# Optimization experiments

Hardware: AMD Instinct MI355X
Metric: run time of the kernel (lower is better)

The kernel has to match this reference:

```python
import jax, jax.numpy as jnp
import numpy as np

D_STATE = 16
D_CONV = 4
EXPAND = 2
GROUPS = 8
EPS = 1e-5


def _layernorm(x, w, b):
    m = x.mean(-1, keepdims=True)
    v = x.var(-1, keepdims=True)
    return (x - m) * jax.lax.rsqrt(v + EPS) * w + b


def _groupnorm(x, w, b):
    B, C = x.shape[:2]
    sp = x.shape[2:]
    xg = x.reshape(B, GROUPS, C // GROUPS, -1)
    m = xg.mean(axis=(2, 3), keepdims=True)
    v = xg.var(axis=(2, 3), keepdims=True)
    xg = (xg - m) * jax.lax.rsqrt(v + EPS)
    x = xg.reshape((B, C) + sp)
    shp = (1, C) + (1,) * len(sp)
    return x * w.reshape(shp) + b.reshape(shp)


def _mamba(xn, in_w, conv_w, conv_b, xp_w, dt_w, dt_b, A_log, Dp, out_w):
    # xn: [B, L, C]
    B, L, C = xn.shape
    di = in_w.shape[0] // 2
    rank = dt_w.shape[1]
    N = D_STATE
    xz = xn @ in_w.T                              # [B, L, 2*di]
    xi, z = xz[..., :di], xz[..., di:]
    # causal depthwise conv1d along L (pad left d_conv-1, truncate to L)
    xc = jnp.moveaxis(xi, 1, 2)                   # [B, di, L]
    xpd = jnp.pad(xc, ((0, 0), (0, 0), (D_CONV - 1, 0)))
    conv = conv_b[None, :, None]
    for k in range(D_CONV):
        conv = conv + conv_w[None, :, k, None] * xpd[:, :, k:k + L]
    u = jnp.moveaxis(jax.nn.silu(conv), 1, 2)     # [B, L, di]
    dbl = u @ xp_w.T                              # [B, L, rank+2N]
    dt = dbl[..., :rank]
    Bm = dbl[..., rank:rank + N]
    Cm = dbl[..., rank + N:]
    delta = jax.nn.softplus(dt @ dt_w.T + dt_b)   # [B, L, di]
    A = -jnp.exp(A_log)                           # [di, N]
    dA = jnp.exp(delta[..., None] * A)            # [B, L, di, N]
    dBu = delta[..., None] * Bm[:, :, None, :] * u[..., None]

    def comb(e1, e2):
        a1, b1 = e1
        a2, b2 = e2
        return a1 * a2, a2 * b1 + b2

    _, h = jax.lax.associative_scan(comb, (dA, dBu), axis=1)  # h_t = dA_t*h_{t-1} + dBu_t
    y = jnp.einsum('bldn,bln->bld', h, Cm) + u * Dp
    y = y * jax.nn.silu(z)
    return y @ out_w.T


def _mamba_layer(x, p):
    B, C = x.shape[:2]
    img = x.shape[2:]
    L = int(np.prod(img))
    xf = jnp.moveaxis(x.reshape(B, C, L), 1, 2)   # [B, L, C]
    xn = _layernorm(xf, p['ln_w'], p['ln_b'])
    xm = _mamba(xn, p['in_w'], p['conv_w'], p['conv_b'], p['xp_w'],
                p['dt_w'], p['dt_b'], p['A_log'], p['Dp'], p['out_w'])
    xm = xm + p['skip'] * xf
    xm = _layernorm(xm, p['ln_w'], p['ln_b'])     # same norm params reused, as in source
    y = xm @ p['proj_w'].T + p['proj_b']
    return jnp.moveaxis(y, 1, 2).reshape((B, C) + img)


def setup_inputs() -> dict:
    key = jax.random.key(0)
    B, C = 2, 48
    img = (16, 32, 32)
    di = EXPAND * C
    rank = -(-C // 16)
    ks = iter(jax.random.split(key, 64))

    def nrm(shape, scale):
        return jax.random.normal(next(ks), shape, jnp.float32) * scale

    inp = {'x': jax.random.normal(next(ks), (B, C) + img, jnp.float32)}
    inp['gn1_w'] = jnp.ones(C); inp['gn1_b'] = jnp.zeros(C)
    inp['gn2_w'] = jnp.ones(C); inp['gn2_b'] = jnp.zeros(C)
    for i in (1, 2):
        inp[f'ln{i}_w'] = jnp.ones(C); inp[f'ln{i}_b'] = jnp.zeros(C)
        inp[f'in_w{i}'] = nrm((2 * di, C), C ** -0.5)
        inp[f'conv_w{i}'] = nrm((di, D_CONV), D_CONV ** -0.5)
        inp[f'conv_b{i}'] = jnp.zeros(di)
        inp[f'xp_w{i}'] = nrm((rank + 2 * D_STATE, di), di ** -0.5)
        inp[f'dt_w{i}'] = nrm((di, rank), rank ** -0.5)
        inp[f'dt_b{i}'] = nrm((di,), 0.1) - 4.0  # softplus -> small positive dt
        inp[f'A_log{i}'] = jnp.log(jnp.tile(jnp.arange(1, D_STATE + 1, dtype=jnp.float32), (di, 1)))
        inp[f'D{i}'] = jnp.ones(di)
        inp[f'out_w{i}'] = nrm((C, di), di ** -0.5)
        inp[f'proj_w{i}'] = nrm((C, C), C ** -0.5)
        inp[f'proj_b{i}'] = jnp.zeros(C)
        inp[f'skip{i}'] = jnp.ones(1)
    return inp


def reference(x, gn1_w, gn1_b, gn2_w, gn2_b,
              ln1_w, ln1_b, in_w1, conv_w1, conv_b1, xp_w1, dt_w1, dt_b1, A_log1, D1, out_w1, proj_w1, proj_b1, skip1,
              ln2_w, ln2_b, in_w2, conv_w2, conv_b2, xp_w2, dt_w2, dt_b2, A_log2, D2, out_w2, proj_w2, proj_b2, skip2):
    p1 = dict(ln_w=ln1_w, ln_b=ln1_b, in_w=in_w1, conv_w=conv_w1, conv_b=conv_b1, xp_w=xp_w1,
              dt_w=dt_w1, dt_b=dt_b1, A_log=A_log1, Dp=D1, out_w=out_w1, proj_w=proj_w1,
              proj_b=proj_b1, skip=skip1)
    p2 = dict(ln_w=ln2_w, ln_b=ln2_b, in_w=in_w2, conv_w=conv_w2, conv_b=conv_b2, xp_w=xp_w2,
              dt_w=dt_w2, dt_b=dt_b2, A_log=A_log2, Dp=D2, out_w=out_w2, proj_w=proj_w2,
              proj_b=proj_b2, skip=skip2)
    identity = x
    h = jax.nn.relu(_groupnorm(x, gn1_w, gn1_b))
    h = _mamba_layer(h, p1)
    h = jax.nn.relu(_groupnorm(h, gn2_w, gn2_b))
    h = _mamba_layer(h, p2)
    return h + identity
```

## Files before the change

### kernel.cpp

```cpp
#include <hip/hip_runtime.h>
#include <hip/hip_bf16.h>

#define LCH   48
#define DI    96
#define LSEQ  16384
#define NB    2
#define NPOS  (NB*LSEQ)
#define NSTATE 16
#define CPG   6
#define EPS   1e-5f
#define NC    128
#define CL    128
#define NCHAIN (NB*DI*NSTATE)
#define TS    32

typedef __hip_bfloat16 bf16;

__device__ __forceinline__ float LDW(const void* p, size_t i, bool f32){
    return f32 ? ((const float*)p)[i] : __bfloat162float(((const bf16*)p)[i]);
}

__device__ __forceinline__ float bf2f(unsigned short h){
    union { unsigned int i; float f; } u; u.i = ((unsigned int)h) << 16; return u.f;
}

__device__ __forceinline__ float4 LDW4(const void* p, size_t i4, bool f32){
    if (f32) return ((const float4*)p)[i4];
    ushort4 v = ((const ushort4*)p)[i4];
    return make_float4(bf2f(v.x), bf2f(v.y), bf2f(v.z), bf2f(v.w));
}

__device__ __forceinline__ float row16_sum(float p){
    union { float f; int i; } u, v;
    u.f = p; v.i = __builtin_amdgcn_mov_dpp(u.i, 0x111, 0xf, 0xf, true); p += v.f;
    u.f = p; v.i = __builtin_amdgcn_mov_dpp(u.i, 0x112, 0xf, 0xf, true); p += v.f;
    u.f = p; v.i = __builtin_amdgcn_mov_dpp(u.i, 0x114, 0xf, 0xf, true); p += v.f;
    u.f = p; v.i = __builtin_amdgcn_mov_dpp(u.i, 0x118, 0xf, 0xf, true); p += v.f;
    return p;
}

__global__ void k_flag(const void* gnw, int* flag, float* __restrict__ acc1, float* __restrict__ acc2){
    int t = threadIdx.x;
    if (t == 0){
        const unsigned short* g = (const unsigned short*)gnw;
        flag[0] = (g[0] == 0x3F80) ? 0 : 1;
    }
    if (t < 32){ acc1[t] = 0.f; acc2[t] = 0.f; }
}

__global__ void k_gnpart_x(const void* __restrict__ x, const int* Fg, float* __restrict__ acc){
    const bool f32 = Fg[0];
    int bg = blockIdx.x >> 4, sl = blockIdx.x & 15;
    int b = bg >> 3, g = bg & 7;
    int tid = threadIdx.x;
    float s = 0.f, q = 0.f;
    for (int c = 0; c < CPG; ++c){
        size_t base = (size_t)(b*LCH + g*CPG + c)*LSEQ + sl*1024;
        float4 v = LDW4(x, base/4 + tid, f32);
        s += v.x; q += v.x*v.x;
        s += v.y; q += v.y*v.y;
        s += v.z; q += v.z*v.z;
        s += v.w; q += v.w*v.w;
    }
    __shared__ float ss[256], sq[256];
    ss[tid] = s; sq[tid] = q; __syncthreads();
    for (int st = 128; st > 0; st >>= 1){
        if (tid < st){ ss[tid] += ss[tid+st]; sq[tid] += sq[tid+st]; }
        __syncthreads();
    }
    if (tid == 0){
        atomicAdd(&acc[bg*2],   ss[0]);
        atomicAdd(&acc[bg*2+1], sq[0]);
    }
}

template<int SRC>
__global__ void k_prepin(const void* __restrict__ src, const int* Fg, const float* __restrict__ acc,
                         const void* gnw, const void* gnb, const void* lnw, const void* lnb,
                         const void* __restrict__ inw,
                         float* __restrict__ xf, float* __restrict__ xi, float* __restrict__ z){
    const bool f32 = Fg[0];
    __shared__ float wl[96*52];
    __shared__ float xl[32*52];
    __shared__ float fl[32*52];
    __shared__ float sst[32];
    int tid = threadIdx.x;
    int part = blockIdx.x & 1;
    int pos0 = (blockIdx.x >> 1)*32;
    int b = pos0 >> 14, l0 = pos0 & (LSEQ-1);
    if (tid < 16){
        float mean = acc[tid*2] / (float)(CPG*LSEQ);
        float var  = acc[tid*2+1] / (float)(CPG*LSEQ) - mean*mean;
        sst[tid*2]   = mean;
        sst[tid*2+1] = rsqrtf(var + EPS);
    }
    for (int i = tid; i < 96*12; i += 256){
        int o = i/12, k4 = i - o*12;
        ((float4*)wl)[o*13+k4] = LDW4(inw, (size_t)part*1152 + i, f32);
    }
    if (SRC == 0){
        for (int i = tid; i < 48*32; i += 256){
            int c = i >> 5, p = i & 31;
            xl[p*52+c] = LDW(src, (size_t)(b*LCH+c)*LSEQ + l0 + p, f32);
        }
    } else {
        const float4* ms4 = (const float4*)src;
        for (int i = tid; i < 32*12; i += 256){
            int p = i/12, c4 = i - p*12;
            ((float4*)xl)[p*13+c4] = ms4[(size_t)pos0*12 + i];
        }
    }
    __syncthreads();
    if (tid < 32){
        float* row  = xl + tid*52;
        float* frow = fl + tid*52;
        float s = 0.f, q = 0.f;
        #pragma unroll
        for (int c = 0; c < LCH; ++c){
            int g = c / CPG;
            float mean = sst[(b*8+g)*2], rs = sst[(b*8+g)*2+1];
            float v = row[c];
            v = (v - mean)*rs*LDW(gnw,c,f32) + LDW(gnb,c,f32);
            v = fmaxf(v, 0.f);
            frow[c] = v; s += v; q += v*v;
        }
        float mean = s / (float)LCH;
        float rs = rsqrtf(q/(float)LCH - mean*mean + EPS);
        #pragma unroll
        for (int c = 0; c < LCH; ++c)
            row[c] = (frow[c]-mean)*rs*LDW(lnw,c,f32) + LDW(lnb,c,f32);
    }
    __syncthreads();
    if (part == 0){
        float4* xf4 = (float4*)xf;
        const float4* fl4 = (const float4*)fl;
        for (int i = tid; i < 32*12; i += 256){
            int p = i/12, c4 = i - p*12;
            xf4[(size_t)pos0*12 + i] = fl4[p*13+c4];
        }
    }
    float* dst = part ? z : xi;
    int o  = tid & 31;
    int pg = tid >> 5;
    const float4* wl4 = (const float4*)wl;
    const float4* xl4 = (const float4*)xl;
    float a0[4] = {0.f,0.f,0.f,0.f};
    float a1[4] = {0.f,0.f,0.f,0.f};
    float a2[4] = {0.f,0.f,0.f,0.f};
    #pragma unroll
    for (int k4 = 0; k4 < 12; ++k4){
        float4 w0 = wl4[ o     *13 + k4];
        float4 w1 = wl4[(o+32)*13 + k4];
        float4 w2 = wl4[(o+64)*13 + k4];
        #pragma unroll
        for (int q = 0; q < 4; ++q){
            float4 xv = xl4[(pg*4+q)*13 + k4];
            a0[q] += xv.x*w0.x; a0[q] += xv.y*w0.y; a0[q] += xv.z*w0.z; a0[q] += xv.w*w0.w;
            a1[q] += xv.x*w1.x; a1[q] += xv.y*w1.y; a1[q] += xv.z*w1.z; a1[q] += xv.w*w1.w;
            a2[q] += xv.x*w2.x; a2[q] += xv.y*w2.y; a2[q] += xv.z*w2.z; a2[q] += xv.w*w2.w;
        }
    }
    #pragma unroll
    for (int q = 0; q < 4; ++q){
        size_t pos = (size_t)(pos0 + pg*4 + q);
        dst[pos*DI + o     ] = a0[q];
        dst[pos*DI + o + 32] = a1[q];
        dst[pos*DI + o + 64] = a2[q];
    }
}

__global__ void k_convdbl(const float* __restrict__ xi, const void* cw, const void* cb,
                          const void* __restrict__ xpw, const void* dtw, const void* dtb,
                          const int* Fg, float* __restrict__ u_g, float* __restrict__ BC2,
                          float* __restrict__ delta_g){
    const bool f32 = Fg[0];
    __shared__ float xil[35*100];
    __shared__ float wbc[32*100];
    __shared__ float wdt[3*100];
    __shared__ float cwl[96*4];
    __shared__ float cbl[96];
    __shared__ float dtwl[96*3];
    __shared__ float dtbl[96];
    __shared__ float dtl[32*3];
    int tid = threadIdx.x;
    int pos0 = blockIdx.x*32;
    int l0 = pos0 & (LSEQ-1);

    for (int i = tid; i < 32*24; i += 256){
        int o = i/24, k4 = i - o*24;
        int row = (o & 1) ? (19 + (o>>1)) : (3 + (o>>1));
        ((float4*)wbc)[o*25 + k4] = LDW4(xpw, (size_t)row*24 + k4, f32);
    }
    if (tid < 72){
        int o = tid/24, k4 = tid - o*24;
        ((float4*)wdt)[o*25 + k4] = LDW4(xpw, (size_t)o*24 + k4, f32);
    }
    for (int i = tid; i < 96*4; i += 256) cwl[i] = LDW(cw, i, f32);
    if (tid < 96) cbl[tid] = LDW(cb, tid, f32);
    for (int i = tid; i < 96*3; i += 256) dtwl[i] = LDW(dtw, i, f32);
    if (tid >= 128 && tid < 224) dtbl[tid-128] = LDW(dtb, tid-128, f32);
    {
        float4* xv = (float4*)xil;
        const float4* gx = (const float4*)xi;
        for (int i = tid; i < 35*24; i += 256){
            int p = i/24, k4 = i - p*24;
            float4 v = make_float4(0.f, 0.f, 0.f, 0.f);
            if (l0 + p - 3 >= 0) v = gx[(size_t)(pos0-3+p)*24 + k4];
            xv[p*25 + k4] = v;
        }
    }
    __syncthreads();

    float uu[12];
    #pragma unroll
    for (int r = 0; r < 12; ++r){
        int i = tid + 256*r;
        int j = i/96, d = i - j*96;
        float4 cw4 = ((const float4*)cwl)[d];
        float acc = cbl[d];
        acc += cw4.x*xil[(j+0)*100+d];
        acc += cw4.y*xil[(j+1)*100+d];
        acc += cw4.z*xil[(j+2)*100+d];
        acc += cw4.w*xil[(j+3)*100+d];
        uu[r] = acc / (1.f + __expf(-acc));
    }
    __syncthreads();

    #pragma unroll
    for (int r = 0; r < 12; ++r){
        int i = tid + 256*r;
        int j = i/96, d = i - j*96;
        xil[j*100+d] = uu[r];
        u_g[(size_t)pos0*DI + i] = uu[r];
    }
    __syncthreads();

    {
        int o  = tid & 31;
        int pg = ((tid>>6)<<1) | ((tid>>5)&1);
        const float4* ulv = (const float4*)xil;
        const float4* wv  = (const float4*)wbc;
        float a0=0.f, a1=0.f, a2=0.f, a3=0.f;
        #pragma unroll 4
        for (int k4 = 0; k4 < 24; ++k4){
            float4 u0 = ulv[(pg*4+0)*25 + k4];
            float4 u1 = ulv[(pg*4+1)*25 + k4];
            float4 u2 = ulv[(pg*4+2)*25 + k4];
            float4 u3 = ulv[(pg*4+3)*25 + k4];
            float4 w  = wv[o*25 + k4];
            a0 += u0.x*w.x; a0 += u0.y*w.y; a0 += u0.z*w.z; a0 += u0.w*w.w;
            a1 += u1.x*w.x; a1 += u1.y*w.y; a1 += u1.z*w.z; a1 += u1.w*w.w;
            a2 += u2.x*w.x; a2 += u2.y*w.y; a2 += u2.z*w.z; a2 += u2.w*w.w;
            a3 += u3.x*w.x; a3 += u3.y*w.y; a3 += u3.z*w.z; a3 += u3.w*w.w;
        }
        size_t pb = (size_t)(pos0 + pg*4);
        BC2[(pb+0)*32 + o] = a0;
        BC2[(pb+1)*32 + o] = a1;
        BC2[(pb+2)*32 + o] = a2;
        BC2[(pb+3)*32 + o] = a3;
    }
    if (tid < 96){
        int o = tid >> 5;
        int p = tid & 31;
        const float4* ulv = (const float4*)xil;
        const float4* wv  = (const float4*)wdt;
        float a = 0.f;
        #pragma unroll 4
        for (int k4 = 0; k4 < 24; ++k4){
            float4 uv = ulv[p*25 + k4];
            float4 w  = wv[o*25 + k4];
            a += uv.x*w.x; a += uv.y*w.y; a += uv.z*w.z; a += uv.w*w.w;
        }
        dtl[p*3+o] = a;
    }
    __syncthreads();

    for (int i = tid; i < 32*96; i += 256){
        int p = i/96, d = i - p*96;
        float acc = dtbl[d];
        #pragma unroll
        for (int r = 0; r < 3; ++r) acc += dtl[p*3+r]*dtwl[d*3+r];
        float sp = (acc > 20.f) ? acc : log1pf(__expf(acc));
        delta_g[(size_t)pos0*DI + i] = sp;
    }
}

__global__ void k_scanA(const float* __restrict__ delta, const float* __restrict__ u,
                        const float* __restrict__ BC2, const void* Alog, const int* Fg,
                        float* __restrict__ Pb, float* __restrict__ Sb){
    const bool f32 = Fg[0];
    __shared__ float  dls[2][TS*16];
    __shared__ float  uus[2][TS*16];
    __shared__ float2 bcs[2][TS*16];
    int tid = threadIdx.x;
    int t = blockIdx.x*256 + tid;
    int n = tid & 15;
    int sg0 = blockIdx.x*16;
    int cb2 = sg0/96;
    int d0 = sg0 - cb2*96;
    int b = cb2 & 1, chunk = cb2 >> 1;
    int dloc = tid >> 4;
    int d = d0 + dloc;
    float An = -__expf(LDW(Alog, d*16+n, f32));
    float P = 1.f, S = 0.f;
    int base = b*LSEQ + chunk*CL;
    const float2* BC2v = (const float2*)BC2;
    int si0 = tid >> 4, sj = tid & 15;
    int si1 = si0 + 16;
    float pd0, pd1, pu0, pu1; float2 pb0, pb1;
    auto fetch = [&](int tb){
        pd0 = delta[(size_t)(tb+si0)*DI + d0 + sj];
        pu0 = u    [(size_t)(tb+si0)*DI + d0 + sj];
        pb0 = BC2v [(size_t)(tb+si0)*16 + sj];
        pd1 = delta[(size_t)(tb+si1)*DI + d0 + sj];
        pu1 = u    [(size_t)(tb+si1)*DI + d0 + sj];
        pb1 = BC2v [(size_t)(tb+si1)*16 + sj];
    };
    auto store = [&](int bs){
        dls[bs][tid] = pd0; dls[bs][tid+256] = pd1;
        uus[bs][tid] = pu0; uus[bs][tid+256] = pu1;
        bcs[bs][tid] = pb0; bcs[bs][tid+256] = pb1;
    };
    fetch(base); store(0);
    __syncthreads();
    for (int tile = 0; tile < CL/TS; ++tile){
        int cur = tile & 1;
        if (tile+1 < CL/TS) fetch(base + (tile+1)*TS);
        #pragma unroll
        for (int i = 0; i < TS; ++i){
            float dl = dls[cur][i*16 + dloc];
            float uu = uus[cur][i*16 + dloc];
            float Bn = bcs[cur][i*16 + n].x;
            float a = __expf(dl*An);
            P *= a;
            S = a*S + dl*Bn*uu;
        }
        if (tile+1 < CL/TS) store(1-cur);
        __syncthreads();
    }
    Pb[t] = P; Sb[t] = S;
}

__global__ void k_scanB(const float* __restrict__ Pb, const float* __restrict__ Sb,
                        float* __restrict__ carry){
    int ch = blockIdx.x*blockDim.x + threadIdx.x;
    float c = 0.f;
    for (int cb = 0; cb < NC; cb += 8){
        float P[8], S[8];
        #pragma unroll
        for (int j = 0; j < 8; ++j){
            P[j] = Pb[(size_t)(cb+j)*NCHAIN + ch];
            S[j] = Sb[(size_t)(cb+j)*NCHAIN + ch];
        }
        #pragma unroll
        for (int j = 0; j < 8; ++j){
            carry[(size_t)(cb+j)*NCHAIN + ch] = c;
            c = S[j] + P[j]*c;
        }
    }
}

__global__ void k_scanC(const float* __restrict__ delta, const float* __restrict__ u,
                        const float* __restrict__ BC2, const float* __restrict__ carry,
                        const void* Alog, const int* Fg, float* __restrict__ y){
    const bool f32 = Fg[0];
    __shared__ float  dls[2][TS*16];
    __shared__ float  uus[2][TS*16];
    __shared__ float2 bcs[2][TS*16];
    int tid = threadIdx.x;
    int n = tid & 15;
    int sg0 = blockIdx.x*16;
    int cb2 = sg0/96;
    int d0 = sg0 - cb2*96;
    int b = cb2 & 1, chunk = cb2 >> 1;
    int dloc = tid >> 4;
    int d = d0 + dloc;
    float An = -__expf(LDW(Alog, d*16+n, f32));
    float h = carry[chunk*NCHAIN + (b*DI+d)*NSTATE + n];
    int base = b*LSEQ + chunk*CL;
    const float2* BC2v = (const float2*)BC2;
    int si0 = tid >> 4, sj = tid & 15;
    int si1 = si0 + 16;
    float pd0, pd1, pu0, pu1; float2 pb0, pb1;
    auto fetch = [&](int tb){
        pd0 = delta[(size_t)(tb+si0)*DI + d0 + sj];
        pu0 = u    [(size_t)(tb+si0)*DI + d0 + sj];
        pb0 = BC2v [(size_t)(tb+si0)*16 + sj];
        pd1 = delta[(size_t)(tb+si1)*DI + d0 + sj];
        pu1 = u    [(size_t)(tb+si1)*DI + d0 + sj];
        pb1 = BC2v [(size_t)(tb+si1)*16 + sj];
    };
    auto store = [&](int bs){
        dls[bs][tid] = pd0; dls[bs][tid+256] = pd1;
        uus[bs][tid] = pu0; uus[bs][tid+256] = pu1;
        bcs[bs][tid] = pb0; bcs[bs][tid+256] = pb1;
    };
    fetch(base); store(0);
    __syncthreads();
    for (int tile = 0; tile < CL/TS; ++tile){
        int cur = tile & 1;
        int tb = base + tile*TS;
        if (tile+1 < CL/TS) fetch(base + (tile+1)*TS);
        #pragma unroll
        for (int i = 0; i < TS; ++i){
            float dl = dls[cur][i*16 + dloc];
            float uu = uus[cur][i*16 + dloc];
            float2 bc = bcs[cur][i*16 + n];
            float a = __expf(dl*An);
            h = a*h + dl*bc.x*uu;
            float p = row16_sum(h*bc.y);
            if (n == 15) y[(size_t)(tb+i)*DI + d] = p;
        }
        if (tile+1 < CL/TS) store(1-cur);
        __syncthreads();
    }
}

__global__ void k_outproj(const float* __restrict__ psum, const void* __restrict__ outw,
                          const void* skipv, const void* Dp, const int* Fg,
                          const float* __restrict__ u, const float* __restrict__ zx,
                          const float* __restrict__ xf, float* __restrict__ xm){
    const bool f32 = Fg[0];
    __shared__ float wl[48*100];
    __shared__ float yl[32*100];
    int tid = threadIdx.x;
    int pos0 = blockIdx.x*32;
    for (int i = tid; i < 48*24; i += 256){
        int o = i/24, k4 = i - o*24;
        ((float4*)wl)[o*25+k4] = LDW4(outw, i, f32);
    }
    {
        const float4* ps4 = (const float4*)psum;
        const float4* uu4 = (const float4*)u;
        const float4* zz4 = (const float4*)zx;
        for (int i = tid; i < 32*24; i += 256){
            int p = i/24, k4 = i - p*24;
            float4 pv = ps4[(size_t)pos0*24 + i];
            float4 uv = uu4[(size_t)pos0*24 + i];
            float4 zv = zz4[(size_t)pos0*24 + i];
            float4 Dv = LDW4(Dp, k4, f32);
            float4 y;
            y.x = (pv.x + uv.x*Dv.x) * (zv.x / (1.f + __expf(-zv.x)));
            y.y = (pv.y + uv.y*Dv.y) * (zv.y / (1.f + __expf(-zv.y)));
            y.z = (pv.z + uv.z*Dv.z) * (zv.z / (1.f + __expf(-zv.z)));
            y.w = (pv.w + uv.w*Dv.w) * (zv.w / (1.f + __expf(-zv.w)));
            ((float4*)yl)[p*25+k4] = y;
        }
    }
    __syncthreads();
    float sk = LDW(skipv, 0, f32);
    int os = tid & 63;
    int pofs = tid >> 6;
    const float4* wl4 = (const float4*)wl;
    const float4* yl4 = (const float4*)yl;
    #pragma unroll
    for (int j = 0; j < 2; ++j){
        int p0 = pofs + j*16;
        float a[4] = {0.f,0.f,0.f,0.f};
        if (os < 48){
            #pragma unroll 4
            for (int k4 = 0; k4 < 24; ++k4){
                float4 w = wl4[os*25+k4];
                #pragma unroll
                for (int q = 0; q < 4; ++q){
                    float4 y = yl4[(p0+q*4)*25+k4];
                    a[q] += y.x*w.x; a[q] += y.y*w.y; a[q] += y.z*w.z; a[q] += y.w*w.w;
                }
            }
            #pragma unroll
            for (int q = 0; q < 4; ++q){
                size_t oi = (size_t)(pos0+p0+q*4)*LCH + os;
                xm[oi] = a[q] + sk*xf[oi];
            }
        }
    }
}

template<int FIN>
__global__ void k_lnproj(const float* __restrict__ xm, const void* lnw, const void* lnb,
                         const void* __restrict__ pw, const void* pb, const int* Fg,
                         const void* __restrict__ xres, float* __restrict__ mout,
                         float* __restrict__ acc2, void* __restrict__ outp){
    const bool f32 = Fg[0];
    __shared__ float wp[48*52];
    __shared__ float xl[32*52];
    __shared__ float ol[32*49];
    __shared__ float gs[48], gq[48];
    int tid = threadIdx.x;
    int pos0 = blockIdx.x*32;
    if (FIN == 0 && tid < 48){ gs[tid] = 0.f; gq[tid] = 0.f; }
    for (int i = tid; i < 48*12; i += 256){
        int o = i/12, k4 = i - o*12;
        ((float4*)wp)[o*13+k4] = LDW4(pw, i, f32);
    }
    {
        const float4* xm4 = (const float4*)xm;
        for (int i = tid; i < 32*12; i += 256){
            int p = i/12, c4 = i - p*12;
            ((float4*)xl)[p*13+c4] = xm4[(size_t)pos0*12 + i];
        }
    }
    __syncthreads();
    if (tid < 32){
        float* row = xl + tid*52;
        float s = 0.f, q = 0.f;
        #pragma unroll
        for (int c = 0; c < LCH; ++c){ float v = row[c]; s += v; q += v*v; }
        float mean = s / (float)LCH;
        float rs = rsqrtf(q/(float)LCH - mean*mean + EPS);
        #pragma unroll
        for (int c = 0; c < LCH; ++c)
            row[c] = (row[c]-mean)*rs*LDW(lnw,c,f32) + LDW(lnb,c,f32);
    }
    __syncthreads();
    int os = tid & 63;
    int pofs = tid >> 6;
    float bias = (os < 48) ? LDW(pb, os, f32) : 0.f;
    const float4* wp4 = (const float4*)wp;
    const float4* xl4 = (const float4*)xl;
    float sl = 0.f, ql = 0.f;
    #pragma unroll
    for (int j = 0; j < 2; ++j){
        int p0 = pofs + j*16;
        float a[4];
        #pragma unroll
        for (int q = 0; q < 4; ++q) a[q] = bias;
        if (os < 48){
            #pragma unroll 4
            for (int k4 = 0; k4 < 12; ++k4){
                float4 w = wp4[os*13+k4];
                #pragma unroll
                for (int q = 0; q < 4; ++q){
                    float4 x = xl4[(p0+q*4)*13+k4];
                    a[q] += x.x*w.x; a[q] += x.y*w.y; a[q] += x.z*w.z; a[q] += x.w*w.w;
                }
            }
            #pragma unroll
            for (int q = 0; q < 4; ++q){
                if (FIN == 0){
                    mout[(size_t)(pos0+p0+q*4)*LCH + os] = a[q];
                    sl += a[q]; ql += a[q]*a[q];
                } else {
                    ol[(p0+q*4)*49 + os] = a[q];
                }
            }
        }
    }
    if (FIN == 0){
        if (os < 48){ atomicAdd(&gs[os], sl); atomicAdd(&gq[os], ql); }
        __syncthreads();
        if (tid < 8){
            int b = pos0 >> 14;
            float s = 0.f, q = 0.f;
            #pragma unroll
            for (int c = 0; c < CPG; ++c){ s += gs[tid*CPG+c]; q += gq[tid*CPG+c]; }
            atomicAdd(&acc2[(b*8+tid)*2],   s);
            atomicAdd(&acc2[(b*8+tid)*2+1], q);
        }
    } else {
        __syncthreads();
        int b = pos0 >> 14, l0 = pos0 & (LSEQ-1);
        for (int i = tid; i < 48*32; i += 256){
            int c = i >> 5, p = i & 31;
            size_t gi = (size_t)(b*LCH+c)*LSEQ + l0 + p;
            float v = ol[p*49+c] + LDW(xres, gi, f32);
            if (f32) ((float*)outp)[gi] = v;
            else     ((bf16*)outp)[gi] = __float2bfloat16(v);
        }
    }
}

extern "C" void kernel_launch(void* const* d_in, const int* in_sizes, int n_in,
                              void* d_out, int out_size, void* d_ws, size_t ws_size,
                              hipStream_t stream){
    const void* x = d_in[0];
    auto W = [&](int i){ return (const void*)d_in[i]; };

    float* ws = (float*)d_ws;
    size_t off = 0;
    int*   flag  = (int*)ws;  off += 16;
    float* acc1  = ws + off;  off += 32;
    float* acc2  = ws + off;  off += 32;
    float* xf    = ws + off;  off += (size_t)NPOS*LCH;
    float* xi    = ws + off;  off += (size_t)NPOS*DI;
    float* zb    = ws + off;  off += (size_t)NPOS*DI;
    float* ub    = ws + off;  off += (size_t)NPOS*DI;
    float* BC2   = ws + off;  off += (size_t)NPOS*32;
    float* Pb    = ws + off;  off += (size_t)NC*NCHAIN;
    float* Sb    = ws + off;  off += (size_t)NC*NCHAIN;
    float* carry = ws + off;  off += (size_t)NC*NCHAIN;
    float* delta = ws + off;  off += (size_t)NPOS*DI;
    float* mbuf  = ws + off;  off += (size_t)NPOS*LCH;
    float* ybuf  = xi;
    float* xmbuf = delta;

    k_flag<<<1, 64, 0, stream>>>(W(1), flag, acc1, acc2);

    k_gnpart_x<<<256, 256, 0, stream>>>(x, flag, acc1);
    k_prepin<0><<<2*NPOS/32, 256, 0, stream>>>(x, flag, acc1, W(1), W(2), W(5), W(6), W(7), xf, xi, zb);
    k_convdbl<<<NPOS/32, 256, 0, stream>>>(xi, W(8), W(9), W(10), W(11), W(12), flag, ub, BC2, delta);
    k_scanA<<<NC*NCHAIN/256, 256, 0, stream>>>(delta, ub, BC2, W(13), flag, Pb, Sb);
    k_scanB<<<NCHAIN/256, 256, 0, stream>>>(Pb, Sb, carry);
    k_scanC<<<NC*NCHAIN/256, 256, 0, stream>>>(delta, ub, BC2, carry, W(13), flag, ybuf);
    k_outproj<<<NPOS/32, 256, 0, stream>>>(ybuf, W(15), W(18), W(14), flag, ub, zb, xf, xmbuf);
    k_lnproj<0><<<NPOS/32, 256, 0, stream>>>(xmbuf, W(5), W(6), W(16), W(17), flag, nullptr, mbuf, acc2, nullptr);

    k_prepin<1><<<2*NPOS/32, 256, 0, stream>>>(mbuf, flag, acc2, W(3), W(4), W(19), W(20), W(21), xf, xi, zb);
    k_convdbl<<<NPOS/32, 256, 0, stream>>>(xi, W(22), W(23), W(24), W(25), W(26), flag, ub, BC2, delta);
    k_scanA<<<NC*NCHAIN/256, 256, 0, stream>>>(delta, ub, BC2, W(27), flag, Pb, Sb);
    k_scanB<<<NCHAIN/256, 256, 0, stream>>>(Pb, Sb, carry);
    k_scanC<<<NC*NCHAIN/256, 256, 0, stream>>>(delta, ub, BC2, carry, W(27), flag, ybuf);
    k_outproj<<<NPOS/32, 256, 0, stream>>>(ybuf, W(29), W(32), W(28), flag, ub, zb, xf, xmbuf);
    k_lnproj<1><<<NPOS/32, 256, 0, stream>>>(xmbuf, W(19), W(20), W(30), W(31), flag, x, nullptr, nullptr, d_out);
}
```

Measured before the change: 453.8 us.

## Store scan inputs channel-major and stream them per thread without shared memory

k_convdbl now writes u, delta, B and C transposed, as [batch, channel, L] rows, so each scan thread can read its own sequence with contiguous float4 loads. This replaces the shared-memory double-buffered tiles and block syncs in scanA and scanC. The D*u skip term moves from outproj into scanC, which drops the u read in outproj. The cost is that convdbl's transposed stores are strided per block, and each scan thread now issues its own loads, which could give poorer coalescing across a wavefront.

```diff
diff --git a/kernel.cpp b/kernel.cpp
--- a/kernel.cpp
+++ b/kernel.cpp
@@ -171,8 +171,8 @@
 
 __global__ void k_convdbl(const float* __restrict__ xi, const void* cw, const void* cb,
                           const void* __restrict__ xpw, const void* dtw, const void* dtb,
-                          const int* Fg, float* __restrict__ u_g, float* __restrict__ BC2,
-                          float* __restrict__ delta_g){
+                          const int* Fg, float* __restrict__ uT, float* __restrict__ BT,
+                          float* __restrict__ CT, float* __restrict__ dT){
     const bool f32 = Fg[0];
     __shared__ float xil[35*100];
     __shared__ float wbc[32*100];
@@ -185,6 +185,7 @@
     int tid = threadIdx.x;
     int pos0 = blockIdx.x*32;
     int l0 = pos0 & (LSEQ-1);
+    int b  = pos0 >> 14;
 
     for (int i = tid; i < 32*24; i += 256){
         int o = i/24, k4 = i - o*24;
@@ -231,7 +232,6 @@
         int i = tid + 256*r;
         int j = i/96, d = i - j*96;
         xil[j*100+d] = uu[r];
-        u_g[(size_t)pos0*DI + i] = uu[r];
     }
     __syncthreads();
 
@@ -253,11 +253,9 @@
             a2 += u2.x*w.x; a2 += u2.y*w.y; a2 += u2.z*w.z; a2 += u2.w*w.w;
             a3 += u3.x*w.x; a3 += u3.y*w.y; a3 += u3.z*w.z; a3 += u3.w*w.w;
         }
-        size_t pb = (size_t)(pos0 + pg*4);
-        BC2[(pb+0)*32 + o] = a0;
-        BC2[(pb+1)*32 + o] = a1;
-        BC2[(pb+2)*32 + o] = a2;
-        BC2[(pb+3)*32 + o] = a3;
+        int nn = o >> 1;
+        float* dstT = (o & 1) ? CT : BT;
+        *(float4*)(dstT + (size_t)(b*16+nn)*LSEQ + l0 + pg*4) = make_float4(a0,a1,a2,a3);
     }
     if (tid < 96){
         int o = tid >> 5;
@@ -273,25 +271,26 @@
         }
         dtl[p*3+o] = a;
     }
-    __syncthreads();
-
-    for (int i = tid; i < 32*96; i += 256){
-        int p = i/96, d = i - p*96;
+    for (int i2 = tid; i2 < 96*32; i2 += 256){
+        int d = i2 >> 5, p = i2 & 31;
+        uT[(size_t)(b*96+d)*LSEQ + l0 + p] = xil[p*100+d];
+    }
+    __syncthreads();
+
+    for (int i2 = tid; i2 < 96*32; i2 += 256){
+        int d = i2 >> 5, p = i2 & 31;
         float acc = dtbl[d];
         #pragma unroll
         for (int r = 0; r < 3; ++r) acc += dtl[p*3+r]*dtwl[d*3+r];
         float sp = (acc > 20.f) ? acc : log1pf(__expf(acc));
-        delta_g[(size_t)pos0*DI + i] = sp;
-    }
-}
-
-__global__ void k_scanA(const float* __restrict__ delta, const float* __restrict__ u,
-                        const float* __restrict__ BC2, const void* Alog, const int* Fg,
+        dT[(size_t)(b*96+d)*LSEQ + l0 + p] = sp;
+    }
+}
+
+__global__ void k_scanA(const float* __restrict__ dTg, const float* __restrict__ uTg,
+                        const float* __restrict__ BTg, const void* Alog, const int* Fg,
                         float* __restrict__ Pb, float* __restrict__ Sb){
     const bool f32 = Fg[0];
-    __shared__ float  dls[2][TS*16];
-    __shared__ float  uus[2][TS*16];
-    __shared__ float2 bcs[2][TS*16];
     int tid = threadIdx.x;
     int t = blockIdx.x*256 + tid;
     int n = tid & 15;
@@ -302,41 +301,21 @@
     int dloc = tid >> 4;
     int d = d0 + dloc;
     float An = -__expf(LDW(Alog, d*16+n, f32));
+    const float4* dp = (const float4*)(dTg + (size_t)(b*96+d)*LSEQ + chunk*CL);
+    const float4* up = (const float4*)(uTg + (size_t)(b*96+d)*LSEQ + chunk*CL);
+    const float4* bp = (const float4*)(BTg + (size_t)(b*16+n)*LSEQ + chunk*CL);
     float P = 1.f, S = 0.f;
-    int base = b*LSEQ + chunk*CL;
-    const float2* BC2v = (const float2*)BC2;
-    int si0 = tid >> 4, sj = tid & 15;
-    int si1 = si0 + 16;
-    float pd0, pd1, pu0, pu1; float2 pb0, pb1;
-    auto fetch = [&](int tb){
-        pd0 = delta[(size_t)(tb+si0)*DI + d0 + sj];
-        pu0 = u    [(size_t)(tb+si0)*DI + d0 + sj];
-        pb0 = BC2v [(size_t)(tb+si0)*16 + sj];
-        pd1 = delta[(size_t)(tb+si1)*DI + d0 + sj];
-        pu1 = u    [(size_t)(tb+si1)*DI + d0 + sj];
-        pb1 = BC2v [(size_t)(tb+si1)*16 + sj];
-    };
-    auto store = [&](int bs){
-        dls[bs][tid] = pd0; dls[bs][tid+256] = pd1;
-        uus[bs][tid] = pu0; uus[bs][tid+256] = pu1;
-        bcs[bs][tid] = pb0; bcs[bs][tid+256] = pb1;
-    };
-    fetch(base); store(0);
-    __syncthreads();
-    for (int tile = 0; tile < CL/TS; ++tile){
-        int cur = tile & 1;
-        if (tile+1 < CL/TS) fetch(base + (tile+1)*TS);
-        #pragma unroll
-        for (int i = 0; i < TS; ++i){
-            float dl = dls[cur][i*16 + dloc];
-            float uu = uus[cur][i*16 + dloc];
-            float Bn = bcs[cur][i*16 + n].x;
-            float a = __expf(dl*An);
-            P *= a;
-            S = a*S + dl*Bn*uu;
-        }
-        if (tile+1 < CL/TS) store(1-cur);
-        __syncthreads();
+    float4 dv = dp[0], uv = up[0], bv = bp[0];
+    #pragma unroll 2
+    for (int t4 = 0; t4 < CL/4; ++t4){
+        float4 d2, u2, b2;
+        if (t4+1 < CL/4){ d2 = dp[t4+1]; u2 = up[t4+1]; b2 = bp[t4+1]; }
+        float a;
+        a = __expf(dv.x*An); P *= a; S = a*S + dv.x*bv.x*uv.x;
+        a = __expf(dv.y*An); P *= a; S = a*S + dv.y*bv.y*uv.y;
+        a = __expf(dv.z*An); P *= a; S = a*S + dv.z*bv.z*uv.z;
+        a = __expf(dv.w*An); P *= a; S = a*S + dv.w*bv.w*uv.w;
+        dv = d2; uv = u2; bv = b2;
     }
     Pb[t] = P; Sb[t] = S;
 }
@@ -360,13 +339,11 @@
     }
 }
 
-__global__ void k_scanC(const float* __restrict__ delta, const float* __restrict__ u,
-                        const float* __restrict__ BC2, const float* __restrict__ carry,
-                        const void* Alog, const int* Fg, float* __restrict__ y){
-    const bool f32 = Fg[0];
-    __shared__ float  dls[2][TS*16];
-    __shared__ float  uus[2][TS*16];
-    __shared__ float2 bcs[2][TS*16];
+__global__ void k_scanC(const float* __restrict__ dTg, const float* __restrict__ uTg,
+                        const float* __restrict__ BTg, const float* __restrict__ CTg,
+                        const float* __restrict__ carry, const void* Alog, const void* Dp,
+                        const int* Fg, float* __restrict__ y){
+    const bool f32 = Fg[0];
     int tid = threadIdx.x;
     int n = tid & 15;
     int sg0 = blockIdx.x*16;
@@ -376,49 +353,38 @@
     int dloc = tid >> 4;
     int d = d0 + dloc;
     float An = -__expf(LDW(Alog, d*16+n, f32));
+    float Dpd = LDW(Dp, d, f32);
     float h = carry[chunk*NCHAIN + (b*DI+d)*NSTATE + n];
-    int base = b*LSEQ + chunk*CL;
-    const float2* BC2v = (const float2*)BC2;
-    int si0 = tid >> 4, sj = tid & 15;
-    int si1 = si0 + 16;
-    float pd0, pd1, pu0, pu1; float2 pb0, pb1;
-    auto fetch = [&](int tb){
-        pd0 = delta[(size_t)(tb+si0)*DI + d0 + sj];
-        pu0 = u    [(size_t)(tb+si0)*DI + d0 + sj];
-        pb0 = BC2v [(size_t)(tb+si0)*16 + sj];
-        pd1 = delta[(size_t)(tb+si1)*DI + d0 + sj];
-        pu1 = u    [(size_t)(tb+si1)*DI + d0 + sj];
-        pb1 = BC2v [(size_t)(tb+si1)*16 + sj];
-    };
-    auto store = [&](int bs){
-        dls[bs][tid] = pd0; dls[bs][tid+256] = pd1;
-        uus[bs][tid] = pu0; uus[bs][tid+256] = pu1;
-        bcs[bs][tid] = pb0; bcs[bs][tid+256] = pb1;
-    };
-    fetch(base); store(0);
-    __syncthreads();
-    for (int tile = 0; tile < CL/TS; ++tile){
-        int cur = tile & 1;
-        int tb = base + tile*TS;
-        if (tile+1 < CL/TS) fetch(base + (tile+1)*TS);
-        #pragma unroll
-        for (int i = 0; i < TS; ++i){
-            float dl = dls[cur][i*16 + dloc];
-            float uu = uus[cur][i*16 + dloc];
-            float2 bc = bcs[cur][i*16 + n];
-            float a = __expf(dl*An);
-            h = a*h + dl*bc.x*uu;
-            float p = row16_sum(h*bc.y);
-            if (n == 15) y[(size_t)(tb+i)*DI + d] = p;
-        }
-        if (tile+1 < CL/TS) store(1-cur);
-        __syncthreads();
+    const float4* dp = (const float4*)(dTg + (size_t)(b*96+d)*LSEQ + chunk*CL);
+    const float4* up = (const float4*)(uTg + (size_t)(b*96+d)*LSEQ + chunk*CL);
+    const float4* bp = (const float4*)(BTg + (size_t)(b*16+n)*LSEQ + chunk*CL);
+    const float4* cp = (const float4*)(CTg + (size_t)(b*16+n)*LSEQ + chunk*CL);
+    size_t tbase = (size_t)(b*LSEQ + chunk*CL);
+    float4 dv = dp[0], uv = up[0], bv = bp[0], cv = cp[0];
+    #pragma unroll 2
+    for (int t4 = 0; t4 < CL/4; ++t4){
+        float4 d2, u2, b2, c2;
+        if (t4+1 < CL/4){ d2 = dp[t4+1]; u2 = up[t4+1]; b2 = bp[t4+1]; c2 = cp[t4+1]; }
+        float a, p;
+        a = __expf(dv.x*An); h = a*h + dv.x*bv.x*uv.x;
+        p = row16_sum(h*cv.x);
+        if (n == 15) y[(tbase + t4*4 + 0)*DI + d] = p + uv.x*Dpd;
+        a = __expf(dv.y*An); h = a*h + dv.y*bv.y*uv.y;
+        p = row16_sum(h*cv.y);
+        if (n == 15) y[(tbase + t4*4 + 1)*DI + d] = p + uv.y*Dpd;
+        a = __expf(dv.z*An); h = a*h + dv.z*bv.z*uv.z;
+        p = row16_sum(h*cv.z);
+        if (n == 15) y[(tbase + t4*4 + 2)*DI + d] = p + uv.z*Dpd;
+        a = __expf(dv.w*An); h = a*h + dv.w*bv.w*uv.w;
+        p = row16_sum(h*cv.w);
+        if (n == 15) y[(tbase + t4*4 + 3)*DI + d] = p + uv.w*Dpd;
+        dv = d2; uv = u2; bv = b2; cv = c2;
     }
 }
 
 __global__ void k_outproj(const float* __restrict__ psum, const void* __restrict__ outw,
-                          const void* skipv, const void* Dp, const int* Fg,
-                          const float* __restrict__ u, const float* __restrict__ zx,
+                          const void* skipv, const int* Fg,
+                          const float* __restrict__ zx,
                           const float* __restrict__ xf, float* __restrict__ xm){
     const bool f32 = Fg[0];
     __shared__ float wl[48*100];
@@ -431,19 +397,16 @@
     }
     {
         const float4* ps4 = (const float4*)psum;
-        const float4* uu4 = (const float4*)u;
         const float4* zz4 = (const float4*)zx;
         for (int i = tid; i < 32*24; i += 256){
             int p = i/24, k4 = i - p*24;
             float4 pv = ps4[(size_t)pos0*24 + i];
-            float4 uv = uu4[(size_t)pos0*24 + i];
             float4 zv = zz4[(size_t)pos0*24 + i];
-            float4 Dv = LDW4(Dp, k4, f32);
             float4 y;
-            y.x = (pv.x + uv.x*Dv.x) * (zv.x / (1.f + __expf(-zv.x)));
-            y.y = (pv.y + uv.y*Dv.y) * (zv.y / (1.f + __expf(-zv.y)));
-            y.z = (pv.z + uv.z*Dv.z) * (zv.z / (1.f + __expf(-zv.z)));
-            y.w = (pv.w + uv.w*Dv.w) * (zv.w / (1.f + __expf(-zv.w)));
+            y.x = pv.x * (zv.x / (1.f + __expf(-zv.x)));
+            y.y = pv.y * (zv.y / (1.f + __expf(-zv.y)));
+            y.z = pv.z * (zv.z / (1.f + __expf(-zv.z)));
+            y.w = pv.w * (zv.w / (1.f + __expf(-zv.w)));
             ((float4*)yl)[p*25+k4] = y;
         }
     }
@@ -585,7 +548,8 @@
     float* xi    = ws + off;  off += (size_t)NPOS*DI;
     float* zb    = ws + off;  off += (size_t)NPOS*DI;
     float* ub    = ws + off;  off += (size_t)NPOS*DI;
-    float* BC2   = ws + off;  off += (size_t)NPOS*32;
+    float* Bt    = ws + off;  off += (size_t)NPOS*16;
+    float* Ct    = ws + off;  off += (size_t)NPOS*16;
     float* Pb    = ws + off;  off += (size_t)NC*NCHAIN;
     float* Sb    = ws + off;  off += (size_t)NC*NCHAIN;
     float* carry = ws + off;  off += (size_t)NC*NCHAIN;
@@ -598,18 +562,18 @@
 
     k_gnpart_x<<<256, 256, 0, stream>>>(x, flag, acc1);
     k_prepin<0><<<2*NPOS/32, 256, 0, stream>>>(x, flag, acc1, W(1), W(2), W(5), W(6), W(7), xf, xi, zb);
-    k_convdbl<<<NPOS/32, 256, 0, stream>>>(xi, W(8), W(9), W(10), W(11), W(12), flag, ub, BC2, delta);
-    k_scanA<<<NC*NCHAIN/256, 256, 0, stream>>>(delta, ub, BC2, W(13), flag, Pb, Sb);
+    k_convdbl<<<NPOS/32, 256, 0, stream>>>(xi, W(8), W(9), W(10), W(11), W(12), flag, ub, Bt, Ct, delta);
+    k_scanA<<<NC*NCHAIN/256, 256, 0, stream>>>(delta, ub, Bt, W(13), flag, Pb, Sb);
     k_scanB<<<NCHAIN/256, 256, 0, stream>>>(Pb, Sb, carry);
-    k_scanC<<<NC*NCHAIN/256, 256, 0, stream>>>(delta, ub, BC2, carry, W(13), flag, ybuf);
-    k_outproj<<<NPOS/32, 256, 0, stream>>>(ybuf, W(15), W(18), W(14), flag, ub, zb, xf, xmbuf);
+    k_scanC<<<NC*NCHAIN/256, 256, 0, stream>>>(delta, ub, Bt, Ct, carry, W(13), W(14), flag, ybuf);
+    k_outproj<<<NPOS/32, 256, 0, stream>>>(ybuf, W(15), W(18), flag, zb, xf, xmbuf);
     k_lnproj<0><<<NPOS/32, 256, 0, stream>>>(xmbuf, W(5), W(6), W(16), W(17), flag, nullptr, mbuf, acc2, nullptr);
 
     k_prepin<1><<<2*NPOS/32, 256, 0, stream>>>(mbuf, flag, acc2, W(3), W(4), W(19), W(20), W(21), xf, xi, zb);
-    k_convdbl<<<NPOS/32, 256, 0, stream>>>(xi, W(22), W(23), W(24), W(25), W(26), flag, ub, BC2, delta);
-    k_scanA<<<NC*NCHAIN/256, 256, 0, stream>>>(delta, ub, BC2, W(27), flag, Pb, Sb);
+    k_convdbl<<<NPOS/32, 256, 0, stream>>>(xi, W(22), W(23), W(24), W(25), W(26), flag, ub, Bt, Ct, delta);
+    k_scanA<<<NC*NCHAIN/256, 256, 0, stream>>>(delta, ub, Bt, W(27), flag, Pb, Sb);
     k_scanB<<<NCHAIN/256, 256, 0, stream>>>(Pb, Sb, carry);
-    k_scanC<<<NC*NCHAIN/256, 256, 0, stream>>>(delta, ub, BC2, carry, W(27), flag, ybuf);
-    k_outproj<<<NPOS/32, 256, 0, stream>>>(ybuf, W(29), W(32), W(28), flag, ub, zb, xf, xmbuf);
+    k_scanC<<<NC*NCHAIN/256, 256, 0, stream>>>(delta, ub, Bt, Ct, carry, W(27), W(28), flag, ybuf);
+    k_outproj<<<NPOS/32, 256, 0, stream>>>(ybuf, W(29), W(32), flag, zb, xf, xmbuf);
     k_lnproj<1><<<NPOS/32, 256, 0, stream>>>(xmbuf, W(19), W(20), W(30), W(31), flag, x, nullptr, nullptr, d_out);
 }
```

New measurement: 544.1 us. 1.2x slower.

## Split B/C into separate buffers, fuse D skip into scan, reorder GEMM loops

Applied to the files above, without the earlier changes.

The interleaved BC2 buffer becomes separate B and C arrays, so scanA reads only B and no longer fetches the unused C half. The u*D skip term moves into scanC's output write, which removes the u and D loads from the out-projection kernel. In outproj and lnproj the j and k loops are swapped so each weight float4 is loaded once and used for both position groups, at the cost of holding more accumulators in registers.

```diff
diff --git a/kernel.cpp b/kernel.cpp
--- a/kernel.cpp
+++ b/kernel.cpp
@@ -171,8 +171,8 @@
 
 __global__ void k_convdbl(const float* __restrict__ xi, const void* cw, const void* cb,
                           const void* __restrict__ xpw, const void* dtw, const void* dtb,
-                          const int* Fg, float* __restrict__ u_g, float* __restrict__ BC2,
-                          float* __restrict__ delta_g){
+                          const int* Fg, float* __restrict__ u_g, float* __restrict__ B2,
+                          float* __restrict__ C2, float* __restrict__ delta_g){
     const bool f32 = Fg[0];
     __shared__ float xil[35*100];
     __shared__ float wbc[32*100];
@@ -253,11 +253,13 @@
             a2 += u2.x*w.x; a2 += u2.y*w.y; a2 += u2.z*w.z; a2 += u2.w*w.w;
             a3 += u3.x*w.x; a3 += u3.y*w.y; a3 += u3.z*w.z; a3 += u3.w*w.w;
         }
+        int nn = o >> 1;
+        float* dst = (o & 1) ? C2 : B2;
         size_t pb = (size_t)(pos0 + pg*4);
-        BC2[(pb+0)*32 + o] = a0;
-        BC2[(pb+1)*32 + o] = a1;
-        BC2[(pb+2)*32 + o] = a2;
-        BC2[(pb+3)*32 + o] = a3;
+        dst[(pb+0)*16 + nn] = a0;
+        dst[(pb+1)*16 + nn] = a1;
+        dst[(pb+2)*16 + nn] = a2;
+        dst[(pb+3)*16 + nn] = a3;
     }
     if (tid < 96){
         int o = tid >> 5;
@@ -286,12 +288,12 @@
 }
 
 __global__ void k_scanA(const float* __restrict__ delta, const float* __restrict__ u,
-                        const float* __restrict__ BC2, const void* Alog, const int* Fg,
+                        const float* __restrict__ B2, const void* Alog, const int* Fg,
                         float* __restrict__ Pb, float* __restrict__ Sb){
     const bool f32 = Fg[0];
-    __shared__ float  dls[2][TS*16];
-    __shared__ float  uus[2][TS*16];
-    __shared__ float2 bcs[2][TS*16];
+    __shared__ float dls[2][TS*16];
+    __shared__ float uus[2][TS*16];
+    __shared__ float bbs[2][TS*16];
     int tid = threadIdx.x;
     int t = blockIdx.x*256 + tid;
     int n = tid & 15;
@@ -304,22 +306,21 @@
     float An = -__expf(LDW(Alog, d*16+n, f32));
     float P = 1.f, S = 0.f;
     int base = b*LSEQ + chunk*CL;
-    const float2* BC2v = (const float2*)BC2;
     int si0 = tid >> 4, sj = tid & 15;
     int si1 = si0 + 16;
-    float pd0, pd1, pu0, pu1; float2 pb0, pb1;
+    float pd0, pd1, pu0, pu1, pb0, pb1;
     auto fetch = [&](int tb){
         pd0 = delta[(size_t)(tb+si0)*DI + d0 + sj];
         pu0 = u    [(size_t)(tb+si0)*DI + d0 + sj];
-        pb0 = BC2v [(size_t)(tb+si0)*16 + sj];
+        pb0 = B2   [(size_t)(tb+si0)*16 + sj];
         pd1 = delta[(size_t)(tb+si1)*DI + d0 + sj];
         pu1 = u    [(size_t)(tb+si1)*DI + d0 + sj];
-        pb1 = BC2v [(size_t)(tb+si1)*16 + sj];
+        pb1 = B2   [(size_t)(tb+si1)*16 + sj];
     };
     auto store = [&](int bs){
         dls[bs][tid] = pd0; dls[bs][tid+256] = pd1;
         uus[bs][tid] = pu0; uus[bs][tid+256] = pu1;
-        bcs[bs][tid] = pb0; bcs[bs][tid+256] = pb1;
+        bbs[bs][tid] = pb0; bbs[bs][tid+256] = pb1;
     };
     fetch(base); store(0);
     __syncthreads();
@@ -330,7 +331,7 @@
         for (int i = 0; i < TS; ++i){
             float dl = dls[cur][i*16 + dloc];
             float uu = uus[cur][i*16 + dloc];
-            float Bn = bcs[cur][i*16 + n].x;
+            float Bn = bbs[cur][i*16 + n];
             float a = __expf(dl*An);
             P *= a;
             S = a*S + dl*Bn*uu;
@@ -361,12 +362,14 @@
 }
 
 __global__ void k_scanC(const float* __restrict__ delta, const float* __restrict__ u,
-                        const float* __restrict__ BC2, const float* __restrict__ carry,
-                        const void* Alog, const int* Fg, float* __restrict__ y){
+                        const float* __restrict__ B2, const float* __restrict__ C2,
+                        const float* __restrict__ carry, const void* Alog, const void* Dp,
+                        const int* Fg, float* __restrict__ y){
     const bool f32 = Fg[0];
-    __shared__ float  dls[2][TS*16];
-    __shared__ float  uus[2][TS*16];
-    __shared__ float2 bcs[2][TS*16];
+    __shared__ float dls[2][TS*16];
+    __shared__ float uus[2][TS*16];
+    __shared__ float bbs[2][TS*16];
+    __shared__ float ccs[2][TS*16];
     int tid = threadIdx.x;
     int n = tid & 15;
     int sg0 = blockIdx.x*16;
@@ -376,24 +379,27 @@
     int dloc = tid >> 4;
     int d = d0 + dloc;
     float An = -__expf(LDW(Alog, d*16+n, f32));
+    float Dpd = LDW(Dp, d, f32);
     float h = carry[chunk*NCHAIN + (b*DI+d)*NSTATE + n];
     int base = b*LSEQ + chunk*CL;
-    const float2* BC2v = (const float2*)BC2;
     int si0 = tid >> 4, sj = tid & 15;
     int si1 = si0 + 16;
-    float pd0, pd1, pu0, pu1; float2 pb0, pb1;
+    float pd0, pd1, pu0, pu1, pb0, pb1, pc0, pc1;
     auto fetch = [&](int tb){
         pd0 = delta[(size_t)(tb+si0)*DI + d0 + sj];
         pu0 = u    [(size_t)(tb+si0)*DI + d0 + sj];
-        pb0 = BC2v [(size_t)(tb+si0)*16 + sj];
+        pb0 = B2   [(size_t)(tb+si0)*16 + sj];
+        pc0 = C2   [(size_t)(tb+si0)*16 + sj];
         pd1 = delta[(size_t)(tb+si1)*DI + d0 + sj];
         pu1 = u    [(size_t)(tb+si1)*DI + d0 + sj];
-        pb1 = BC2v [(size_t)(tb+si1)*16 + sj];
+        pb1 = B2   [(size_t)(tb+si1)*16 + sj];
+        pc1 = C2   [(size_t)(tb+si1)*16 + sj];
     };
     auto store = [&](int bs){
         dls[bs][tid] = pd0; dls[bs][tid+256] = pd1;
         uus[bs][tid] = pu0; uus[bs][tid+256] = pu1;
-        bcs[bs][tid] = pb0; bcs[bs][tid+256] = pb1;
+        bbs[bs][tid] = pb0; bbs[bs][tid+256] = pb1;
+        ccs[bs][tid] = pc0; ccs[bs][tid+256] = pc1;
     };
     fetch(base); store(0);
     __syncthreads();
@@ -405,11 +411,12 @@
         for (int i = 0; i < TS; ++i){
             float dl = dls[cur][i*16 + dloc];
             float uu = uus[cur][i*16 + dloc];
-            float2 bc = bcs[cur][i*16 + n];
+            float Bn = bbs[cur][i*16 + n];
+            float Cn = ccs[cur][i*16 + n];
             float a = __expf(dl*An);
-            h = a*h + dl*bc.x*uu;
-            float p = row16_sum(h*bc.y);
-            if (n == 15) y[(size_t)(tb+i)*DI + d] = p;
+            h = a*h + dl*Bn*uu;
+            float p = row16_sum(h*Cn);
+            if (n == 15) y[(size_t)(tb+i)*DI + d] = p + uu*Dpd;
         }
         if (tile+1 < CL/TS) store(1-cur);
         __syncthreads();
@@ -417,8 +424,8 @@
 }
 
 __global__ void k_outproj(const float* __restrict__ psum, const void* __restrict__ outw,
-                          const void* skipv, const void* Dp, const int* Fg,
-                          const float* __restrict__ u, const float* __restrict__ zx,
+                          const void* skipv, const int* Fg,
+                          const float* __restrict__ zx,
                           const float* __restrict__ xf, float* __restrict__ xm){
     const bool f32 = Fg[0];
     __shared__ float wl[48*100];
@@ -431,19 +438,16 @@
     }
     {
         const float4* ps4 = (const float4*)psum;
-        const float4* uu4 = (const float4*)u;
         const float4* zz4 = (const float4*)zx;
         for (int i = tid; i < 32*24; i += 256){
             int p = i/24, k4 = i - p*24;
             float4 pv = ps4[(size_t)pos0*24 + i];
-            float4 uv = uu4[(size_t)pos0*24 + i];
             float4 zv = zz4[(size_t)pos0*24 + i];
-            float4 Dv = LDW4(Dp, k4, f32);
             float4 y;
-            y.x = (pv.x + uv.x*Dv.x) * (zv.x / (1.f + __expf(-zv.x)));
-            y.y = (pv.y + uv.y*Dv.y) * (zv.y / (1.f + __expf(-zv.y)));
-            y.z = (pv.z + uv.z*Dv.z) * (zv.z / (1.f + __expf(-zv.z)));
-            y.w = (pv.w + uv.w*Dv.w) * (zv.w / (1.f + __expf(-zv.w)));
+            y.x = pv.x * (zv.x / (1.f + __expf(-zv.x)));
+            y.y = pv.y * (zv.y / (1.f + __expf(-zv.y)));
+            y.z = pv.z * (zv.z / (1.f + __expf(-zv.z)));
+            y.w = pv.w * (zv.w / (1.f + __expf(-zv.w)));
             ((float4*)yl)[p*25+k4] = y;
         }
     }
@@ -453,24 +457,28 @@
     int pofs = tid >> 6;
     const float4* wl4 = (const float4*)wl;
     const float4* yl4 = (const float4*)yl;
-    #pragma unroll
-    for (int j = 0; j < 2; ++j){
-        int p0 = pofs + j*16;
-        float a[4] = {0.f,0.f,0.f,0.f};
-        if (os < 48){
-            #pragma unroll 4
-            for (int k4 = 0; k4 < 24; ++k4){
-                float4 w = wl4[os*25+k4];
+    float a[2][4] = {{0.f,0.f,0.f,0.f},{0.f,0.f,0.f,0.f}};
+    if (os < 48){
+        #pragma unroll 4
+        for (int k4 = 0; k4 < 24; ++k4){
+            float4 w = wl4[os*25+k4];
+            #pragma unroll
+            for (int j = 0; j < 2; ++j){
+                int p0 = pofs + j*16;
                 #pragma unroll
                 for (int q = 0; q < 4; ++q){
                     float4 y = yl4[(p0+q*4)*25+k4];
-                    a[q] += y.x*w.x; a[q] += y.y*w.y; a[q] += y.z*w.z; a[q] += y.w*w.w;
+                    a[j][q] += y.x*w.x; a[j][q] += y.y*w.y; a[j][q] += y.z*w.z; a[j][q] += y.w*w.w;
                 }
             }
+        }
+        #pragma unroll
+        for (int j = 0; j < 2; ++j){
+            int p0 = pofs + j*16;
             #pragma unroll
             for (int q = 0; q < 4; ++q){
                 size_t oi = (size_t)(pos0+p0+q*4)*LCH + os;
-                xm[oi] = a[q] + sk*xf[oi];
+                xm[oi] = a[j][q] + sk*xf[oi];
             }
         }
     }
@@ -519,29 +527,31 @@
     const float4* wp4 = (const float4*)wp;
     const float4* xl4 = (const float4*)xl;
     float sl = 0.f, ql = 0.f;
-    #pragma unroll
-    for (int j = 0; j < 2; ++j){
-        int p0 = pofs + j*16;
-        float a[4];
-        #pragma unroll
-        for (int q = 0; q < 4; ++q) a[q] = bias;
-        if (os < 48){
-            #pragma unroll 4
-            for (int k4 = 0; k4 < 12; ++k4){
-                float4 w = wp4[os*13+k4];
+    float a[2][4] = {{bias,bias,bias,bias},{bias,bias,bias,bias}};
+    if (os < 48){
+        #pragma unroll 4
+        for (int k4 = 0; k4 < 12; ++k4){
+            float4 w = wp4[os*13+k4];
+            #pragma unroll
+            for (int j = 0; j < 2; ++j){
+                int p0 = pofs + j*16;
                 #pragma unroll
                 for (int q = 0; q < 4; ++q){
                     float4 x = xl4[(p0+q*4)*13+k4];
-                    a[q] += x.x*w.x; a[q] += x.y*w.y; a[q] += x.z*w.z; a[q] += x.w*w.w;
+                    a[j][q] += x.x*w.x; a[j][q] += x.y*w.y; a[j][q] += x.z*w.z; a[j][q] += x.w*w.w;
                 }
             }
+        }
+        #pragma unroll
+        for (int j = 0; j < 2; ++j){
+            int p0 = pofs + j*16;
             #pragma unroll
             for (int q = 0; q < 4; ++q){
                 if (FIN == 0){
-                    mout[(size_t)(pos0+p0+q*4)*LCH + os] = a[q];
-                    sl += a[q]; ql += a[q]*a[q];
+                    mout[(size_t)(pos0+p0+q*4)*LCH + os] = a[j][q];
+                    sl += a[j][q]; ql += a[j][q]*a[j][q];
                 } else {
-                    ol[(p0+q*4)*49 + os] = a[q];
+                    ol[(p0+q*4)*49 + os] = a[j][q];
                 }
             }
         }
@@ -585,7 +595,8 @@
     float* xi    = ws + off;  off += (size_t)NPOS*DI;
     float* zb    = ws + off;  off += (size_t)NPOS*DI;
     float* ub    = ws + off;  off += (size_t)NPOS*DI;
-    float* BC2   = ws + off;  off += (size_t)NPOS*32;
+    float* B2    = ws + off;  off += (size_t)NPOS*16;
+    float* C2    = ws + off;  off += (size_t)NPOS*16;
     float* Pb    = ws + off;  off += (size_t)NC*NCHAIN;
     float* Sb    = ws + off;  off += (size_t)NC*NCHAIN;
     float* carry = ws + off;  off += (size_t)NC*NCHAIN;
@@ -598,18 +609,18 @@
 
     k_gnpart_x<<<256, 256, 0, stream>>>(x, flag, acc1);
     k_prepin<0><<<2*NPOS/32, 256, 0, stream>>>(x, flag, acc1, W(1), W(2), W(5), W(6), W(7), xf, xi, zb);
-    k_convdbl<<<NPOS/32, 256, 0, stream>>>(xi, W(8), W(9), W(10), W(11), W(12), flag, ub, BC2, delta);
-    k_scanA<<<NC*NCHAIN/256, 256, 0, stream>>>(delta, ub, BC2, W(13), flag, Pb, Sb);
+    k_convdbl<<<NPOS/32, 256, 0, stream>>>(xi, W(8), W(9), W(10), W(11), W(12), flag, ub, B2, C2, delta);
+    k_scanA<<<NC*NCHAIN/256, 256, 0, stream>>>(delta, ub, B2, W(13), flag, Pb, Sb);
     k_scanB<<<NCHAIN/256, 256, 0, stream>>>(Pb, Sb, carry);
-    k_scanC<<<NC*NCHAIN/256, 256, 0, stream>>>(delta, ub, BC2, carry, W(13), flag, ybuf);
-    k_outproj<<<NPOS/32, 256, 0, stream>>>(ybuf, W(15), W(18), W(14), flag, ub, zb, xf, xmbuf);
+    k_scanC<<<NC*NCHAIN/256, 256, 0, stream>>>(delta, ub, B2, C2, carry, W(13), W(14), flag, ybuf);
+    k_outproj<<<NPOS/32, 256, 0, stream>>>(ybuf, W(15), W(18), flag, zb, xf, xmbuf);
     k_lnproj<0><<<NPOS/32, 256, 0, stream>>>(xmbuf, W(5), W(6), W(16), W(17), flag, nullptr, mbuf, acc2, nullptr);
 
     k_prepin<1><<<2*NPOS/32, 256, 0, stream>>>(mbuf, flag, acc2, W(3), W(4), W(19), W(20), W(21), xf, xi, zb);
-    k_convdbl<<<NPOS/32, 256, 0, stream>>>(xi, W(22), W(23), W(24), W(25), W(26), flag, ub, BC2, delta);
-    k_scanA<<<NC*NCHAIN/256, 256, 0, stream>>>(delta, ub, BC2, W(27), flag, Pb, Sb);
+    k_convdbl<<<NPOS/32, 256, 0, stream>>>(xi, W(22), W(23), W(24), W(25), W(26), flag, ub, B2, C2, delta);
+    k_scanA<<<NC*NCHAIN/256, 256, 0, stream>>>(delta, ub, B2, W(27), flag, Pb, Sb);
     k_scanB<<<NCHAIN/256, 256, 0, stream>>>(Pb, Sb, carry);
-    k_scanC<<<NC*NCHAIN/256, 256, 0, stream>>>(delta, ub, BC2, carry, W(27), flag, ybuf);
-    k_outproj<<<NPOS/32, 256, 0, stream>>>(ybuf, W(29), W(32), W(28), flag, ub, zb, xf, xmbuf);
+    k_scanC<<<NC*NCHAIN/256, 256, 0, stream>>>(delta, ub, B2, C2, carry, W(27), W(28), flag, ybuf);
+    k_outproj<<<NPOS/32, 256, 0, stream>>>(ybuf, W(29), W(32), flag, zb, xf, xmbuf);
     k_lnproj<1><<<NPOS/32, 256, 0, stream>>>(xmbuf, W(19), W(20), W(30), W(31), flag, x, nullptr, nullptr, d_out);
 }
```

After: 446.2 us. Within noise of the previous version (-1.7%).
